# Performance work log

Hardware: AMD Instinct MI355X
Metric: run time of the kernel (lower is better)

## Reference

```python
import jax, jax.numpy as jnp
import numpy as np

DIM, NWIN, TOPK, HEADS = 128, 8, 4, 4
SCALE = DIM ** -0.5


def conv2d(x, w, groups=1, pad=0):
    return jax.lax.conv_general_dilated(
        x, w, (1, 1), [(pad, pad), (pad, pad)],
        feature_group_count=groups,
        dimension_numbers=('NCHW', 'OIHW', 'NCHW'))


def to_windows(elem):
    # elem: [b, C, H, W] -> [b, n_hw, hs, ws, C]
    b, c, h, w = elem.shape
    hs, ws = h // NWIN, w // NWIN
    y = elem.transpose(0, 2, 3, 1)                       # b H W C
    y = y.reshape(b, NWIN, hs, NWIN, ws, c)
    y = y.transpose(0, 1, 3, 2, 4, 5)                    # b n_h n_w hs ws C
    return y.reshape(b, NWIN * NWIN, hs, ws, c)


def from_windows(out, hs, ws):
    # out: [b, n_hw, s_hw, C] -> [b, H, W, C]
    b, nw, s, c = out.shape
    y = out.reshape(b, NWIN, NWIN, hs, ws, c)
    y = y.transpose(0, 1, 3, 2, 4, 5)
    return y.reshape(b, NWIN * hs, NWIN * ws, c)


def window_attention(elem, mlp_w, mlp_b):
    # elem: [b, 3*dim, H, W]
    b, c3, h, w = elem.shape
    hs, ws = h // NWIN, w // NWIN
    win = to_windows(elem)                               # b n_hw hs ws 3C
    q = win[..., :DIM]                                   # b n_hw hs ws C
    kv = win[..., DIM:]                                  # b n_hw hs ws 2C
    nw, s = NWIN * NWIN, hs * ws
    q_pix = q.reshape(b, nw, s, DIM)
    kv_pix = kv.reshape(b, nw, s, 2 * DIM)
    # window-level 'max' projection (WinProj)
    q_win = jax.lax.stop_gradient(q_pix.max(axis=2))             # b nw C
    k_win = jax.lax.stop_gradient(kv_pix[..., :DIM].max(axis=2))  # b nw C
    # top-k routing (diff_routing=False, mul_weight='none' -> only indices used)
    logits = jnp.einsum('bic,bjc->bij', q_win * SCALE, k_win)    # b nw nw
    _, r_idx = jax.lax.top_k(logits, TOPK)                       # b nw topk
    # gather selected kv windows: b nw topk s 2C
    kv_sel = jax.vmap(lambda kvb, ib: kvb[ib])(kv_pix, r_idx)
    kv_sel = kv_sel.reshape(b, nw, TOPK * s, 2 * DIM)
    k_sel = kv_sel[..., :DIM].reshape(b, nw, TOPK * s, HEADS, DIM // HEADS)
    v_sel = kv_sel[..., DIM:].reshape(b, nw, TOPK * s, HEADS, DIM // HEADS)
    qh = q_pix.reshape(b, nw, s, HEADS, DIM // HEADS)
    attn = jnp.einsum('bwshd,bwthd->bwhst', qh * SCALE, k_sel)
    attn = jax.nn.softmax(attn, axis=-1)
    out = jnp.einsum('bwhst,bwthd->bwshd', attn, v_sel)
    out = out.reshape(b, nw, s, DIM)
    out = from_windows(out, hs, ws)                      # b H W C
    out = jnp.einsum('bhwi,oi->bhwo', out, mlp_w) + mlp_b
    return out.transpose(0, 3, 1, 2)                     # b C H W


def setup_inputs() -> dict:
    key = jax.random.key(0)
    ks = jax.random.split(key, 12)
    d = DIM
    return {
        'x': jax.random.normal(ks[0], (1, d, 128, 128), jnp.float32),
        'qkv2_w': jax.random.normal(ks[1], (3 * d, d, 1, 1), jnp.float32) * 0.05,
        'dw3_w': jax.random.normal(ks[2], (3 * d, 1, 3, 3), jnp.float32) * 0.1,
        'pw3_w': jax.random.normal(ks[3], (3 * d, (3 * d) // (3 * HEADS), 1, 1), jnp.float32) * 0.05,
        'dw5_w': jax.random.normal(ks[4], (3 * d, 1, 5, 5), jnp.float32) * 0.1,
        'pw5_w': jax.random.normal(ks[5], (3 * d, (3 * d) // (3 * HEADS), 1, 1), jnp.float32) * 0.05,
        'mlp_w': jax.random.normal(ks[6], (d, d), jnp.float32) * 0.05,
        'mlp_b': jnp.zeros((d,), jnp.float32),
        'proj_w': jax.random.normal(ks[7], (d, 3 * d, 1, 1), jnp.float32) * 0.05,
        'ln_g': jnp.ones((d,), jnp.float32),
        'ln_b': jnp.zeros((d,), jnp.float32),
    }


def reference(x, qkv2_w, dw3_w, pw3_w, dw5_w, pw5_w, mlp_w, mlp_b, proj_w, ln_g, ln_b):
    qkv = conv2d(x, qkv2_w)                              # b 3C H W
    branches = [qkv]
    for dw, pw, k in ((dw3_w, pw3_w, 3), (dw5_w, pw5_w, 5)):
        y = conv2d(qkv, dw, groups=3 * DIM, pad=k // 2)  # depthwise
        y = conv2d(y, pw, groups=3 * HEADS)              # grouped 1x1
        branches.append(y)
    outs = [window_attention(e, mlp_w, mlp_b) for e in branches]
    out = jnp.concatenate(outs, axis=1)                  # b 3C H W
    out = conv2d(out, proj_w)                            # b C H W
    # ln2d: LayerNorm over channel dim
    mu = out.mean(axis=1, keepdims=True)
    var = out.var(axis=1, keepdims=True)
    out = (out - mu) * jax.lax.rsqrt(var + 1e-5)
    out = out * ln_g[None, :, None, None] + ln_b[None, :, None, None]
    return out
```

## Files before the change

kernel.cpp:

```cpp
#include <hip/hip_runtime.h>
#include <math.h>

#define P 16384
#define SCALEF 0.08838834764831845f
#define QSCALE 0.12752075616290145f

typedef short bf16x8 __attribute__((ext_vector_type(8)));
typedef float f32x4 __attribute__((ext_vector_type(4)));

__device__ __forceinline__ unsigned short f2bf(float x) {
  union { float f; unsigned int u; } v; v.f = x;
  unsigned int r = v.u + 0x7fffu + ((v.u >> 16) & 1u);
  return (unsigned short)(r >> 16);
}
__device__ __forceinline__ unsigned int packbf(float a, float b) {
  return (unsigned int)f2bf(a) | ((unsigned int)f2bf(b) << 16);
}
__device__ __forceinline__ unsigned int pr2(float a, float b) {
  union { float f; unsigned int u; } ua, ub; ua.f = a; ub.f = b;
  return __builtin_amdgcn_perm(ub.u + 0x8000u, ua.u + 0x8000u, 0x07060302u);
}
__device__ __forceinline__ unsigned int pk2(float a, float b) {
  unsigned int r;
  asm("v_cvt_pk_bf16_f32 %0, %1, %2" : "=v"(r) : "v"(a), "v"(b));
  return r;
}
#define EXP2F(x) __builtin_amdgcn_exp2f(x)

template<int NS, int JT>
__global__ __launch_bounds__(256) void k_conv_mfma(
    const float* __restrict__ in, const float* __restrict__ w,
    const float* __restrict__ bias, float* __restrict__ out,
    const int IC, const int in_zstr, const int out_zstr)
{
  const int p0  = blockIdx.x * (JT * 64);
  const int oc0 = blockIdx.y * 64;
  in  += (size_t)blockIdx.z * (size_t)in_zstr;
  out += (size_t)blockIdx.z * (size_t)out_zstr;
  const int tid = threadIdx.x;
  const int wv = tid >> 6;
  const int lane = tid & 63;
  const int qi = lane & 15, g = lane >> 4;

  __shared__ __align__(16) unsigned int bS[NS][JT * 64 * 16];
  __shared__ __align__(16) unsigned int aS[NS][64 * 16];

  const f32x4 fz = {0.f, 0.f, 0.f, 0.f};
  f32x4 acc[JT][4];
  #pragma unroll
  for (int j = 0; j < JT; ++j)
    #pragma unroll
    for (int o = 0; o < 4; ++o) acc[j][o] = fz;

  for (int k0 = 0; k0 < IC; k0 += 32) {
    __syncthreads();
    {
      const int kB = tid >> 4;
      const int pB = (tid & 15) * (JT * 4);
      const float* r0 = in + (size_t)(k0 + 2 * kB) * P + p0 + pB;
      #pragma unroll
      for (int half = 0; half < JT / 2; ++half) {
        float x0[8], x1[8];
        #pragma unroll
        for (int v = 0; v < 2; ++v) {
          float4 a = ((const float4*)r0)[half * 2 + v];
          float4 c = ((const float4*)(r0 + P))[half * 2 + v];
          x0[4*v] = a.x; x0[4*v+1] = a.y; x0[4*v+2] = a.z; x0[4*v+3] = a.w;
          x1[4*v] = c.x; x1[4*v+1] = c.y; x1[4*v+2] = c.z; x1[4*v+3] = c.w;
        }
        #pragma unroll
        for (int ii = 0; ii < 8; ++ii) {
          const int i8 = (ii + tid) & 7;
          const int i = half * 8 + i8;
          const unsigned idx = (unsigned)((pB + i) * 16 + (kB ^ ((i & 3) << 2)));
          const unsigned u0 = __float_as_uint(x0[i8]);
          const unsigned u1 = __float_as_uint(x1[i8]);
          bS[0][idx] = __builtin_amdgcn_perm(u1, u0, 0x07060302u);
          const float r0f = x0[i8] - __uint_as_float(u0 & 0xffff0000u);
          const float r1f = x1[i8] - __uint_as_float(u1 & 0xffff0000u);
          bS[1][idx] = pr2(r0f, r1f);
        }
      }
    }
    {
      const int oA = tid >> 2;
      const int kA = (tid & 3) * 8;
      const float* rw = w + (size_t)(oc0 + oA) * IC + k0 + kA;
      float4 wa = ((const float4*)rw)[0];
      float4 wb = ((const float4*)rw)[1];
      float y[8] = {wa.x, wa.y, wa.z, wa.w, wb.x, wb.y, wb.z, wb.w};
      #pragma unroll
      for (int i = 0; i < 4; ++i) {
        const int dd = (kA >> 1) + i;
        const unsigned idx = (unsigned)(oA * 16 + (dd ^ ((oA & 3) << 2)));
        const unsigned u0 = __float_as_uint(y[2*i]);
        const unsigned u1 = __float_as_uint(y[2*i+1]);
        aS[0][idx] = __builtin_amdgcn_perm(u1, u0, 0x07060302u);
        const float r0f = y[2*i]   - __uint_as_float(u0 & 0xffff0000u);
        const float r1f = y[2*i+1] - __uint_as_float(u1 & 0xffff0000u);
        aS[1][idx] = pr2(r0f, r1f);
      }
    }
    __syncthreads();

    bf16x8 aF[4][NS];
    #pragma unroll
    for (int o = 0; o < 4; ++o) {
      const unsigned ab = (unsigned)((o * 16 + qi) * 16 + 4 * (g ^ (qi & 3)));
      #pragma unroll
      for (int s = 0; s < NS; ++s)
        aF[o][s] = *(const bf16x8*)&aS[s][ab];
    }
    #pragma unroll
    for (int j = 0; j < JT; ++j) {
      const unsigned bb = (unsigned)(((wv * JT + j) * 16 + qi) * 16 + 4 * (g ^ (qi & 3)));
      const bf16x8 b0 = *(const bf16x8*)&bS[0][bb];
      const bf16x8 b1 = *(const bf16x8*)&bS[1][bb];
      #pragma unroll
      for (int o = 0; o < 4; ++o) {
        acc[j][o] = __builtin_amdgcn_mfma_f32_16x16x32_bf16(aF[o][0], b0, acc[j][o], 0, 0, 0);
        acc[j][o] = __builtin_amdgcn_mfma_f32_16x16x32_bf16(aF[o][0], b1, acc[j][o], 0, 0, 0);
        acc[j][o] = __builtin_amdgcn_mfma_f32_16x16x32_bf16(aF[o][1], b0, acc[j][o], 0, 0, 0);
      }
    }
  }

  float bv[4][4];
  #pragma unroll
  for (int o = 0; o < 4; ++o)
    #pragma unroll
    for (int t = 0; t < 4; ++t)
      bv[o][t] = bias ? bias[oc0 + o * 16 + 4 * g + t] : 0.f;

  #pragma unroll
  for (int j = 0; j < JT; ++j) {
    const int px = p0 + (wv * JT + j) * 16 + qi;
    #pragma unroll
    for (int o = 0; o < 4; ++o)
      #pragma unroll
      for (int t = 0; t < 4; ++t)
        out[(size_t)(oc0 + o * 16 + 4 * g + t) * P + px] = acc[j][o][t] + bv[o][t];
  }
}

__global__ __launch_bounds__(256) void k_projln(
    const float* __restrict__ in, const float* __restrict__ w,
    const float* __restrict__ bias, const float* __restrict__ ln_g,
    const float* __restrict__ ln_b, float* __restrict__ out)
{
  const int p0 = blockIdx.x * 64;
  const int tid = threadIdx.x;
  const int wv = tid >> 6;
  const int lane = tid & 63;
  const int qi = lane & 15, g = lane >> 4;

  __shared__ __align__(16) unsigned int bS[2][64 * 16];
  __shared__ __align__(16) unsigned int aS[2][128 * 16];

  const f32x4 fz = {0.f, 0.f, 0.f, 0.f};
  f32x4 acc[8];
  #pragma unroll
  for (int o = 0; o < 8; ++o) acc[o] = fz;

  for (int k0 = 0; k0 < 384; k0 += 32) {
    __syncthreads();
    {
      const int kB = tid >> 4;
      const int pB = (tid & 15) * 4;
      const float* r0 = in + (size_t)(k0 + 2 * kB) * P + p0 + pB;
      float4 a = *(const float4*)r0;
      float4 c = *(const float4*)(r0 + P);
      const float x0[4] = {a.x, a.y, a.z, a.w};
      const float x1[4] = {c.x, c.y, c.z, c.w};
      #pragma unroll
      for (int i = 0; i < 4; ++i) {
        const unsigned idx = (unsigned)((pB + i) * 16 + (kB ^ (i << 2)));
        const unsigned u0 = __float_as_uint(x0[i]);
        const unsigned u1 = __float_as_uint(x1[i]);
        bS[0][idx] = __builtin_amdgcn_perm(u1, u0, 0x07060302u);
        const float r0f = x0[i] - __uint_as_float(u0 & 0xffff0000u);
        const float r1f = x1[i] - __uint_as_float(u1 & 0xffff0000u);
        bS[1][idx] = pr2(r0f, r1f);
      }
    }
    {
      const int oA = tid >> 1;
      const int kA = (tid & 1) * 16;
      const float* rw = w + (size_t)oA * 384 + k0 + kA;
      float4 wa = ((const float4*)rw)[0];
      float4 wb = ((const float4*)rw)[1];
      float4 wc = ((const float4*)rw)[2];
      float4 wd = ((const float4*)rw)[3];
      const float y[16] = {wa.x, wa.y, wa.z, wa.w, wb.x, wb.y, wb.z, wb.w,
                           wc.x, wc.y, wc.z, wc.w, wd.x, wd.y, wd.z, wd.w};
      #pragma unroll
      for (int i = 0; i < 8; ++i) {
        const int dd = (kA >> 1) + i;
        const unsigned idx = (unsigned)(oA * 16 + (dd ^ ((oA & 3) << 2)));
        const unsigned u0 = __float_as_uint(y[2*i]);
        const unsigned u1 = __float_as_uint(y[2*i+1]);
        aS[0][idx] = __builtin_amdgcn_perm(u1, u0, 0x07060302u);
        const float r0f = y[2*i]   - __uint_as_float(u0 & 0xffff0000u);
        const float r1f = y[2*i+1] - __uint_as_float(u1 & 0xffff0000u);
        aS[1][idx] = pr2(r0f, r1f);
      }
    }
    __syncthreads();

    const unsigned bb = (unsigned)((wv * 16 + qi) * 16 + 4 * (g ^ (qi & 3)));
    const bf16x8 b0 = *(const bf16x8*)&bS[0][bb];
    const bf16x8 b1 = *(const bf16x8*)&bS[1][bb];
    #pragma unroll
    for (int o = 0; o < 8; ++o) {
      const unsigned ab = (unsigned)((o * 16 + qi) * 16 + 4 * (g ^ (qi & 3)));
      const bf16x8 a0 = *(const bf16x8*)&aS[0][ab];
      const bf16x8 a1 = *(const bf16x8*)&aS[1][ab];
      acc[o] = __builtin_amdgcn_mfma_f32_16x16x32_bf16(a0, b0, acc[o], 0, 0, 0);
      acc[o] = __builtin_amdgcn_mfma_f32_16x16x32_bf16(a0, b1, acc[o], 0, 0, 0);
      acc[o] = __builtin_amdgcn_mfma_f32_16x16x32_bf16(a1, b0, acc[o], 0, 0, 0);
    }
  }

  const int px = p0 + wv * 16 + qi;
  float vch[8][4];
  float sum = 0.f, sq = 0.f;
  #pragma unroll
  for (int o = 0; o < 8; ++o)
    #pragma unroll
    for (int t = 0; t < 4; ++t) {
      const float v = acc[o][t] + bias[o * 16 + 4 * g + t];
      vch[o][t] = v; sum += v; sq += v * v;
    }
  sum += __shfl_xor(sum, 16, 64); sum += __shfl_xor(sum, 32, 64);
  sq  += __shfl_xor(sq, 16, 64);  sq  += __shfl_xor(sq, 32, 64);
  const float mu = sum * (1.f / 128.f);
  const float var = sq * (1.f / 128.f) - mu * mu;
  const float rs = rsqrtf(var + 1e-5f);
  #pragma unroll
  for (int o = 0; o < 8; ++o)
    #pragma unroll
    for (int t = 0; t < 4; ++t) {
      const int oc = o * 16 + 4 * g + t;
      out[(size_t)oc * P + px] = (vch[o][t] - mu) * rs * ln_g[oc] + ln_b[oc];
    }
}

__global__ __launch_bounds__(128) void k_fold(
    const float* __restrict__ proj_w, const float* __restrict__ mlp_w,
    const float* __restrict__ mlp_b, float* __restrict__ Wc,
    float* __restrict__ bc)
{
  const int o = blockIdx.x;
  const int b = blockIdx.y;
  const int i = threadIdx.x;
  const float* pw = proj_w + o * 384 + b * 128;
  float acc = 0.f;
  for (int j = 0; j < 128; ++j)
    acc += pw[j] * mlp_w[j * 128 + i];
  Wc[o * 384 + b * 128 + i] = acc;
  if (b == 0) {
    const float* pwo = proj_w + o * 384;
    float s = (pwo[i] + pwo[i + 128] + pwo[i + 256]) * mlp_b[i];
    #pragma unroll
    for (int sh = 1; sh <= 32; sh <<= 1) s += __shfl_xor(s, sh, 64);
    __shared__ float r2[2];
    if ((i & 63) == 0) r2[i >> 6] = s;
    __syncthreads();
    if (i == 0) bc[o] = r2[0] + r2[1];
  }
}

__global__ __launch_bounds__(256) void k_dwf(
    const float* __restrict__ in, const float* __restrict__ w3,
    const float* __restrict__ w5, float* __restrict__ out3,
    float* __restrict__ out5)
{
  const int c  = blockIdx.y;
  const int ty = blockIdx.x;
  const int y0 = ty * 16;
  __shared__ float tS[20][136];
  const float* ip = in + (size_t)c * P;

  if (threadIdx.x < 20) {
    tS[threadIdx.x][0] = 0.f; tS[threadIdx.x][1] = 0.f;
    tS[threadIdx.x][130] = 0.f; tS[threadIdx.x][131] = 0.f;
  }
  for (int e = threadIdx.x; e < 640; e += 256) {
    const int r = e >> 5, q = e & 31;
    const int gy = y0 + r - 2;
    float4 v = make_float4(0.f, 0.f, 0.f, 0.f);
    if (gy >= 0 && gy < 128) v = *(const float4*)&ip[gy * 128 + q * 4];
    *(float4*)&tS[r][2 + q * 4] = v;
  }
  __syncthreads();

  float a3[9], a5[25];
  #pragma unroll
  for (int i = 0; i < 9; ++i)  a3[i] = w3[c * 9 + i];
  #pragma unroll
  for (int i = 0; i < 25; ++i) a5[i] = w5[c * 25 + i];

  const int py  = threadIdx.x >> 4;
  const int px0 = (threadIdx.x & 15) * 8;
  float o3[8] = {}, o5[8] = {};
  #pragma unroll
  for (int r = 0; r < 5; ++r) {
    float4 sa = *(const float4*)&tS[py + r][px0];
    float4 sb = *(const float4*)&tS[py + r][px0 + 4];
    float4 sc = *(const float4*)&tS[py + r][px0 + 8];
    const float s[12] = {sa.x, sa.y, sa.z, sa.w, sb.x, sb.y, sb.z, sb.w,
                         sc.x, sc.y, sc.z, sc.w};
    #pragma unroll
    for (int j = 0; j < 8; ++j) {
      float acc = a5[r * 5 + 0] * s[j];
      #pragma unroll
      for (int d = 1; d < 5; ++d) acc += a5[r * 5 + d] * s[j + d];
      o5[j] += acc;
    }
    if (r >= 1 && r <= 3) {
      #pragma unroll
      for (int j = 0; j < 8; ++j) {
        float b = a3[(r - 1) * 3 + 0] * s[j + 1];
        b += a3[(r - 1) * 3 + 1] * s[j + 2];
        b += a3[(r - 1) * 3 + 2] * s[j + 3];
        o3[j] += b;
      }
    }
  }
  const size_t ob = (size_t)c * P + (y0 + py) * 128 + px0;
  float4* p3 = (float4*)&out3[ob];
  float4* p5 = (float4*)&out5[ob];
  p3[0] = make_float4(o3[0], o3[1], o3[2], o3[3]);
  p3[1] = make_float4(o3[4], o3[5], o3[6], o3[7]);
  p5[0] = make_float4(o5[0], o5[1], o5[2], o5[3]);
  p5[1] = make_float4(o5[4], o5[5], o5[6], o5[7]);
}

__global__ __launch_bounds__(256) void k_pw2(
    const float* in0, const float* __restrict__ w0, float* out0,
    const float* in1, const float* __restrict__ w1, float* out1)
{
  const float* in = blockIdx.z ? in1 : in0;
  const float* w  = blockIdx.z ? w1 : w0;
  float*      out = blockIdx.z ? out1 : out0;
  const int g = blockIdx.y;
  const int p = blockIdx.x * 256 + threadIdx.x;
  __shared__ float wL[1024];
  for (int e = threadIdx.x; e < 1024; e += 256) wL[e] = w[g * 1024 + e];
  __syncthreads();
  float r[32];
  #pragma unroll
  for (int i = 0; i < 32; ++i) r[i] = in[(g * 32 + i) * P + p];
  #pragma unroll
  for (int o = 0; o < 32; ++o) {
    float acc = 0.f;
    #pragma unroll
    for (int i = 0; i < 32; ++i) acc += wL[o * 32 + i] * r[i];
    out[(g * 32 + o) * P + p] = acc;
  }
}

__global__ __launch_bounds__(256) void k_topk(
    const float* __restrict__ qwin, const float* __restrict__ kwin,
    int* __restrict__ ridx)
{
  const int b = blockIdx.y;
  const int i = blockIdx.x * 4 + (threadIdx.x >> 6);
  const int j = threadIdx.x & 63;
  const float4* q4 = (const float4*)&qwin[(b * 64 + i) * 128];
  const float4* k4 = (const float4*)&kwin[(b * 64 + j) * 128];
  float v = 0.f;
  #pragma unroll
  for (int t = 0; t < 32; ++t) {
    float4 a = q4[t], c = k4[t];
    v += a.x * c.x + a.y * c.y + a.z * c.z + a.w * c.w;
  }
  int res[4];
  #pragma unroll
  for (int r = 0; r < 4; ++r) {
    float bv = v; int bj = j;
    #pragma unroll
    for (int s = 1; s < 64; s <<= 1) {
      const float ov = __shfl_xor(bv, s, 64);
      const int   oj = __shfl_xor(bj, s, 64);
      if (ov > bv || (ov == bv && oj < bj)) { bv = ov; bj = oj; }
    }
    res[r] = bj;
    if (j == bj) v = -INFINITY;
  }
  if (j == 0)
    *(int4*)&ridx[(b * 64 + i) * 4] = make_int4(res[0], res[1], res[2], res[3]);
}

__global__ __launch_bounds__(256) void k_repack(
    const float* __restrict__ e0, const float* __restrict__ e1,
    const float* __restrict__ e2, unsigned int* __restrict__ kvimg,
    unsigned int* __restrict__ qimg, float* __restrict__ qwin,
    float* __restrict__ kwin)
{
  const int fl = blockIdx.x + 64 * (blockIdx.y + 4 * blockIdx.z);
  const int nf = (fl & 7) * 96 + (fl >> 3);
  const int w = nf & 63, h = (nf >> 6) & 3, b = nf >> 8;
  const float* e = (b == 0) ? e0 : ((b == 1) ? e1 : e2);
  const int wy = w >> 3, wx = w & 7;
  const int jbase = wy * 16 * 128 + wx * 16;
  const int t = threadIdx.x;
  unsigned int* kwin_img = kvimg + (size_t)((b * 4 + h) * 64 + w) * 8192;
  unsigned int* qwin_img = qimg  + (size_t)((b * 4 + h) * 64 + w) * 4096;

  __shared__ float redS[32][257];
  __shared__ float part[8][32];
  float kreg[32];

  {
    const int key = t;
    const int hw = jbase + (key >> 4) * 128 + (key & 15);
    const float* eK = e + (size_t)(128 + h * 32) * P + hw;
    const float* eQ = e + (size_t)(h * 32) * P + hw;
    const int half = key >> 7, kl = key & 127;
    unsigned int* kd = kwin_img + half * 4096 + kl * 16;
    unsigned int* qd = qwin_img + key * 16;
    #pragma unroll
    for (int dd = 0; dd < 16; ++dd) {
      float k0 = eK[(size_t)(2 * dd) * P], k1 = eK[(size_t)(2 * dd + 1) * P];
      kd[dd ^ ((kl & 3) << 2)] = packbf(k0, k1);
      kreg[2 * dd] = k0; kreg[2 * dd + 1] = k1;
      float q0 = eQ[(size_t)(2 * dd) * P];
      float q1 = eQ[(size_t)(2 * dd + 1) * P];
      redS[2 * dd][key] = q0; redS[2 * dd + 1][key] = q1;
      qd[dd] = packbf(q0 * QSCALE, q1 * QSCALE);
    }
  }
  {
    const int half = t >> 7, tt = t & 127;
    const int d = tt >> 2;
    const int kp0 = (tt & 3) * 16;
    const float* eV = e + (size_t)(256 + h * 32 + d) * P;
    unsigned int* vd = kwin_img + half * 4096 + 2048 + d * 64;
    #pragma unroll
    for (int i = 0; i < 16; ++i) {
      const int kp2 = kp0 + i;
      const int key = half * 128 + kp2 * 2;
      const int hw = jbase + (key >> 4) * 128 + (key & 15);
      float v0 = eV[hw], v1 = eV[hw + 1];
      vd[kp2 ^ ((d & 7) << 2)] = packbf(v0, v1);
    }
  }
  __syncthreads();
  {
    const int ch = t & 31, seg = t >> 5;
    float mx = redS[ch][seg * 32];
    #pragma unroll
    for (int i = 1; i < 32; ++i) mx = fmaxf(mx, redS[ch][seg * 32 + i]);
    part[seg][ch] = mx;
  }
  __syncthreads();
  if (t < 32) {
    float mx = part[0][t];
    #pragma unroll
    for (int s = 1; s < 8; ++s) mx = fmaxf(mx, part[s][t]);
    qwin[(size_t)(b * 64 + w) * 128 + h * 32 + t] = mx;
  }
  #pragma unroll
  for (int d = 0; d < 32; ++d) redS[d][t] = kreg[d];
  __syncthreads();
  {
    const int ch = t & 31, seg = t >> 5;
    float mx = redS[ch][seg * 32];
    #pragma unroll
    for (int i = 1; i < 32; ++i) mx = fmaxf(mx, redS[ch][seg * 32 + i]);
    part[seg][ch] = mx;
  }
  __syncthreads();
  if (t < 32) {
    float mx = part[0][t];
    #pragma unroll
    for (int s = 1; s < 8; ++s) mx = fmaxf(mx, part[s][t]);
    kwin[(size_t)(b * 64 + w) * 128 + h * 32 + t] = mx;
  }
}

__global__ __launch_bounds__(512, 4) void k_attn_mfma(
    const unsigned int* __restrict__ kvimg, const unsigned int* __restrict__ qimg,
    const int* __restrict__ ridx, float* __restrict__ attnch)
{
  const int fl = blockIdx.x + 64 * (blockIdx.y + 4 * blockIdx.z);
  const int nf = (fl & 7) * 96 + (fl >> 3);
  const int w = nf & 63, h = (nf >> 6) & 3, b = nf >> 8;
  const int tid = threadIdx.x;
  const int wv = tid >> 6, lane = tid & 63;
  const int qi = lane & 15, g = lane >> 4;
  const int wy = w >> 3, wx = w & 7;

  __shared__ __align__(16) unsigned int kvbuf[2][4096];

  const unsigned int* kwin = kvimg + (size_t)((b * 4 + h) * 64) * 8192;
  const unsigned int* qwin = qimg + (size_t)((b * 4 + h) * 64 + w) * 4096;

  bf16x8 qv[2];
  #pragma unroll
  for (int s = 0; s < 2; ++s) {
    union { uint4 u; bf16x8 v; } tq;
    tq.u = *(const uint4*)(qwin + ((wv * 2 + s) * 16 + qi) * 16 + g * 4);
    qv[s] = tq.v;
  }
  const int4 jv = *(const int4*)(ridx + (b * 64 + w) * 4);
  const int ja[4] = {jv.x, jv.y, jv.z, jv.w};

  const f32x4 fz = {0.f, 0.f, 0.f, 0.f};
  float m[2], l[2];
  f32x4 acc[2][2];
  #pragma unroll
  for (int s = 0; s < 2; ++s) {
    m[s] = -3.0e38f; l[s] = 0.f; acc[s][0] = fz; acc[s][1] = fz;
  }

  uint4 st0, st1;
  {
    const uint4* s4 = (const uint4*)(kwin + (size_t)ja[0] * 8192);
    st0 = s4[tid]; st1 = s4[512 + tid];
  }

#define SOFTMAX_PACK(SC, S, PB) {                                           \
    float wmax = -3.0e38f;                                                  \
    _Pragma("unroll") for (int c = 0; c < 4; ++c)                           \
      _Pragma("unroll") for (int u = 0; u < 2; ++u)                         \
        _Pragma("unroll") for (int t2 = 0; t2 < 4; ++t2)                    \
          wmax = fmaxf(wmax, SC[c][u][t2]);                                 \
    wmax = fmaxf(wmax, __shfl_xor(wmax, 16, 64));                           \
    wmax = fmaxf(wmax, __shfl_xor(wmax, 32, 64));                           \
    const float mnew = fmaxf(m[S], wmax);                                   \
    const float corr = EXP2F(m[S] - mnew);                                  \
    m[S] = mnew;                                                            \
    acc[S][0] *= corr; acc[S][1] *= corr;                                   \
    float psum = 0.f;                                                       \
    _Pragma("unroll") for (int c = 0; c < 4; ++c)                           \
      _Pragma("unroll") for (int u = 0; u < 2; ++u) {                       \
        const float p0 = EXP2F(SC[c][u][0] - mnew);                         \
        const float p1 = EXP2F(SC[c][u][1] - mnew);                         \
        const float p2 = EXP2F(SC[c][u][2] - mnew);                         \
        const float p3 = EXP2F(SC[c][u][3] - mnew);                         \
        psum += (p0 + p1) + (p2 + p3);                                      \
        PB[c][2 * u]     = pk2(p0, p1);                                     \
        PB[c][2 * u + 1] = pk2(p2, p3);                                     \
      }                                                                     \
    l[S] = l[S] * corr + psum;                                              \
  }

  for (int ch = 0; ch < 8; ++ch) {
    {
      uint4* d4 = (uint4*)kvbuf[ch & 1];
      d4[tid] = st0; d4[512 + tid] = st1;
    }
    if (ch < 7) {
      const int nx = ch + 1;
      const uint4* s4 = (const uint4*)(kwin + (size_t)ja[nx >> 1] * 8192
                                       + (size_t)(nx & 1) * 4096);
      st0 = s4[tid]; st1 = s4[512 + tid];
    }
    __syncthreads();

    const unsigned int* bc = kvbuf[ch & 1];
    const bf16x8* kp = (const bf16x8*)bc;
    const unsigned short* vsh = (const unsigned short*)(bc + 2048);

    f32x4 scA[4][2], scB[4][2];
    __builtin_amdgcn_s_setprio(1);
    #pragma unroll
    for (int c = 0; c < 4; ++c) {
      #pragma unroll
      for (int u = 0; u < 2; ++u) {
        const int key = 32 * c + 8 * (qi >> 2) + 4 * u + (qi & 3);
        const bf16x8 ka = kp[key * 4 + (g ^ (qi & 3))];
        scA[c][u] = __builtin_amdgcn_mfma_f32_16x16x32_bf16(ka, qv[0], fz, 0, 0, 0);
        scB[c][u] = __builtin_amdgcn_mfma_f32_16x16x32_bf16(ka, qv[1], fz, 0, 0, 0);
      }
    }
    __builtin_amdgcn_s_setprio(0);
    unsigned int pbA[4][4], pbB[4][4];
    SOFTMAX_PACK(scA, 0, pbA);
    SOFTMAX_PACK(scB, 1, pbB);
    __builtin_amdgcn_s_setprio(1);
    #pragma unroll
    for (int c = 0; c < 4; ++c) {
      #pragma unroll
      for (int dt = 0; dt < 2; ++dt) {
        const int d0 = dt * 16 + qi;
        const bf16x8 va = *(const bf16x8*)&vsh[
            (unsigned)((d0 * 128 + 32 * c + 8 * g) ^ ((d0 & 7) << 3))];
        union { unsigned int u4[4]; bf16x8 v; } pva, pvb;
        pva.u4[0] = pbA[c][0]; pva.u4[1] = pbA[c][1];
        pva.u4[2] = pbA[c][2]; pva.u4[3] = pbA[c][3];
        pvb.u4[0] = pbB[c][0]; pvb.u4[1] = pbB[c][1];
        pvb.u4[2] = pbB[c][2]; pvb.u4[3] = pbB[c][3];
        acc[0][dt] = __builtin_amdgcn_mfma_f32_16x16x32_bf16(va, pva.v, acc[0][dt], 0, 0, 0);
        acc[1][dt] = __builtin_amdgcn_mfma_f32_16x16x32_bf16(va, pvb.v, acc[1][dt], 0, 0, 0);
      }
    }
    __builtin_amdgcn_s_setprio(0);
  }
#undef SOFTMAX_PACK

  #pragma unroll
  for (int s = 0; s < 2; ++s) {
    float lsum = l[s];
    lsum += __shfl_xor(lsum, 16, 64);
    lsum += __shfl_xor(lsum, 32, 64);
    const float inv = 1.f / lsum;
    const int hwq = (wy * 16 + wv * 2 + s) * 128 + wx * 16 + qi;
    #pragma unroll
    for (int dt = 0; dt < 2; ++dt)
      #pragma unroll
      for (int t = 0; t < 4; ++t) {
        const int d = dt * 16 + 4 * g + t;
        attnch[(size_t)(b * 128 + h * 32 + d) * P + hwq] = acc[s][dt][t] * inv;
      }
  }
}

extern "C" void kernel_launch(void* const* d_in, const int* in_sizes, int n_in,
                              void* d_out, int out_size, void* d_ws, size_t ws_size,
                              hipStream_t stream)
{
  (void)in_sizes; (void)n_in; (void)out_size;
  const float* x      = (const float*)d_in[0];
  const float* qkv2_w = (const float*)d_in[1];
  const float* dw3_w  = (const float*)d_in[2];
  const float* pw3_w  = (const float*)d_in[3];
  const float* dw5_w  = (const float*)d_in[4];
  const float* pw5_w  = (const float*)d_in[5];
  const float* mlp_w  = (const float*)d_in[6];
  const float* mlp_b  = (const float*)d_in[7];
  const float* proj_w = (const float*)d_in[8];
  const float* ln_g   = (const float*)d_in[9];
  const float* ln_b   = (const float*)d_in[10];

  float* ws = (float*)d_ws;
  const size_t CH = (size_t)384 * P;
  float* qkv    = ws;
  float* dwt3   = ws + CH;
  float* y3     = ws + 2 * CH;
  float* y5     = ws + 3 * CH;
  float* qwin   = ws + 5 * CH;
  float* kwin   = qwin + 3 * 64 * 128;
  int*   ridx   = (int*)(kwin + 3 * 64 * 128);
  float* Wc     = (float*)(ridx + 768);
  float* bc     = Wc + 128 * 384;
  unsigned int* kvimg = (unsigned int*)(ws + 4 * CH);
  unsigned int* qimg  = (unsigned int*)dwt3;
  float* attnch = y3;
  (void)ws_size;

  k_fold<<<dim3(128, 3), 128, 0, stream>>>(proj_w, mlp_w, mlp_b, Wc, bc);

  k_conv_mfma<2, 2><<<dim3(128, 6, 1), 256, 0, stream>>>(x, qkv2_w, nullptr, qkv, 128, 0, 0);
  k_dwf<<<dim3(8, 384), 256, 0, stream>>>(qkv, dw3_w, dw5_w, dwt3, y5);
  k_pw2<<<dim3(64, 12, 2), 256, 0, stream>>>(dwt3, pw3_w, y3, y5, pw5_w, y5);
  k_repack<<<dim3(64, 4, 3), 256, 0, stream>>>(qkv, y3, y5, kvimg, qimg, qwin, kwin);
  k_topk<<<dim3(16, 3), 256, 0, stream>>>(qwin, kwin, ridx);
  k_attn_mfma<<<dim3(64, 4, 3), 512, 0, stream>>>(kvimg, qimg, ridx, attnch);
  k_projln<<<dim3(256), 256, 0, stream>>>(attnch, Wc, bc, ln_g, ln_b, (float*)d_out);
}
```

Before: 185.3 us.

## Process window pairs in repack for wider coalesced loads; reorder dwf grid

k_repack now has each 512-thread block handle two horizontally adjacent windows. Row reads therefore cover 32 contiguous floats instead of 16, and V is loaded as float4 rows instead of scattered scalar pairs. The max reductions for q and k are staged per window through shared memory in four phases. k_dwf's grid is transposed so consecutive blocks walk channels rather than row tiles, which changes cache and scheduling order. The cost is more barriers, larger register arrays (qreg and kreg) and half as many blocks.

```diff
diff --git a/kernel.cpp b/kernel.cpp
--- a/kernel.cpp
+++ b/kernel.cpp
@@ -275,8 +275,8 @@
     const float* __restrict__ w5, float* __restrict__ out3,
     float* __restrict__ out5)
 {
-  const int c  = blockIdx.y;
-  const int ty = blockIdx.x;
+  const int c  = blockIdx.x;
+  const int ty = blockIdx.y;
   const int y0 = ty * 16;
   __shared__ float tS[20][136];
   const float* ip = in + (size_t)c * P;
@@ -392,91 +392,98 @@
     *(int4*)&ridx[(b * 64 + i) * 4] = make_int4(res[0], res[1], res[2], res[3]);
 }
 
-__global__ __launch_bounds__(256) void k_repack(
+__global__ __launch_bounds__(512) void k_repack(
     const float* __restrict__ e0, const float* __restrict__ e1,
     const float* __restrict__ e2, unsigned int* __restrict__ kvimg,
     unsigned int* __restrict__ qimg, float* __restrict__ qwin,
     float* __restrict__ kwin)
 {
-  const int fl = blockIdx.x + 64 * (blockIdx.y + 4 * blockIdx.z);
-  const int nf = (fl & 7) * 96 + (fl >> 3);
-  const int w = nf & 63, h = (nf >> 6) & 3, b = nf >> 8;
+  const int fl = blockIdx.x + 32 * (blockIdx.y + 4 * blockIdx.z);
+  const int nf = (fl & 7) * 48 + (fl >> 3);
+  const int wp = nf & 31, h = (nf >> 5) & 3, b = nf >> 7;
   const float* e = (b == 0) ? e0 : ((b == 1) ? e1 : e2);
-  const int wy = w >> 3, wx = w & 7;
-  const int jbase = wy * 16 * 128 + wx * 16;
+  const int w0 = wp * 2;
+  const int wy = w0 >> 3, wx0 = w0 & 7;
+  const int jbase0 = (wy * 16) * 128 + wx0 * 16;
   const int t = threadIdx.x;
-  unsigned int* kwin_img = kvimg + (size_t)((b * 4 + h) * 64 + w) * 8192;
-  unsigned int* qwin_img = qimg  + (size_t)((b * 4 + h) * 64 + w) * 4096;
 
   __shared__ float redS[32][257];
-  __shared__ float part[8][32];
-  float kreg[32];
-
+  __shared__ float part[16][32];
+
+  float qreg[32], kreg[32];
+
+  const int row = t >> 5, x = t & 31;
+  const int win = x >> 4, key = row * 16 + (x & 15);
   {
-    const int key = t;
-    const int hw = jbase + (key >> 4) * 128 + (key & 15);
+    const int hw = jbase0 + row * 128 + x;
     const float* eK = e + (size_t)(128 + h * 32) * P + hw;
     const float* eQ = e + (size_t)(h * 32) * P + hw;
     const int half = key >> 7, kl = key & 127;
-    unsigned int* kd = kwin_img + half * 4096 + kl * 16;
-    unsigned int* qd = qwin_img + key * 16;
+    unsigned int* kd = kvimg + (size_t)((b * 4 + h) * 64 + w0 + win) * 8192
+                       + half * 4096 + kl * 16;
+    unsigned int* qd = qimg + (size_t)((b * 4 + h) * 64 + w0 + win) * 4096
+                       + key * 16;
     #pragma unroll
     for (int dd = 0; dd < 16; ++dd) {
       float k0 = eK[(size_t)(2 * dd) * P], k1 = eK[(size_t)(2 * dd + 1) * P];
+      kreg[2 * dd] = k0; kreg[2 * dd + 1] = k1;
       kd[dd ^ ((kl & 3) << 2)] = packbf(k0, k1);
-      kreg[2 * dd] = k0; kreg[2 * dd + 1] = k1;
-      float q0 = eQ[(size_t)(2 * dd) * P];
-      float q1 = eQ[(size_t)(2 * dd + 1) * P];
-      redS[2 * dd][key] = q0; redS[2 * dd + 1][key] = q1;
+      float q0 = eQ[(size_t)(2 * dd) * P], q1 = eQ[(size_t)(2 * dd + 1) * P];
+      qreg[2 * dd] = q0; qreg[2 * dd + 1] = q1;
       qd[dd] = packbf(q0 * QSCALE, q1 * QSCALE);
     }
   }
   {
-    const int half = t >> 7, tt = t & 127;
-    const int d = tt >> 2;
-    const int kp0 = (tt & 3) * 16;
-    const float* eV = e + (size_t)(256 + h * 32 + d) * P;
-    unsigned int* vd = kwin_img + half * 4096 + 2048 + d * 64;
-    #pragma unroll
-    for (int i = 0; i < 16; ++i) {
-      const int kp2 = kp0 + i;
-      const int key = half * 128 + kp2 * 2;
-      const int hw = jbase + (key >> 4) * 128 + (key & 15);
-      float v0 = eV[hw], v1 = eV[hw + 1];
-      vd[kp2 ^ ((d & 7) << 2)] = packbf(v0, v1);
-    }
-  }
-  __syncthreads();
-  {
-    const int ch = t & 31, seg = t >> 5;
-    float mx = redS[ch][seg * 32];
-    #pragma unroll
-    for (int i = 1; i < 32; ++i) mx = fmaxf(mx, redS[ch][seg * 32 + i]);
-    part[seg][ch] = mx;
-  }
-  __syncthreads();
-  if (t < 32) {
-    float mx = part[0][t];
-    #pragma unroll
-    for (int s = 1; s < 8; ++s) mx = fmaxf(mx, part[s][t]);
-    qwin[(size_t)(b * 64 + w) * 128 + h * 32 + t] = mx;
-  }
-  #pragma unroll
-  for (int d = 0; d < 32; ++d) redS[d][t] = kreg[d];
-  __syncthreads();
-  {
-    const int ch = t & 31, seg = t >> 5;
-    float mx = redS[ch][seg * 32];
-    #pragma unroll
-    for (int i = 1; i < 32; ++i) mx = fmaxf(mx, redS[ch][seg * 32 + i]);
-    part[seg][ch] = mx;
-  }
-  __syncthreads();
-  if (t < 32) {
-    float mx = part[0][t];
-    #pragma unroll
-    for (int s = 1; s < 8; ++s) mx = fmaxf(mx, part[s][t]);
-    kwin[(size_t)(b * 64 + w) * 128 + h * 32 + t] = mx;
+    const int vwin = t & 1, r = t >> 1;
+    const int half = r >> 7, d = (r & 127) >> 2, q4 = r & 3;
+    const int R = 8 * half + 2 * q4;
+    const float* eV = e + (size_t)(256 + h * 32 + d) * P + jbase0 + vwin * 16;
+    float rv[2][16];
+    #pragma unroll
+    for (int rr = 0; rr < 2; ++rr) {
+      const float4* src = (const float4*)&eV[(R + rr) * 128];
+      #pragma unroll
+      for (int i = 0; i < 4; ++i) {
+        float4 v = src[i];
+        rv[rr][4*i] = v.x; rv[rr][4*i+1] = v.y;
+        rv[rr][4*i+2] = v.z; rv[rr][4*i+3] = v.w;
+      }
+    }
+    unsigned int* vd = kvimg + (size_t)((b * 4 + h) * 64 + w0 + vwin) * 8192
+                       + half * 4096 + 2048 + d * 64;
+    #pragma unroll
+    for (int j = 0; j < 16; ++j) {
+      const int kp2 = q4 * 16 + j;
+      const int rr = j >> 3, pp = (j & 7) * 2;
+      vd[kp2 ^ ((d & 7) << 2)] = packbf(rv[rr][pp], rv[rr][pp + 1]);
+    }
+  }
+  #pragma unroll
+  for (int ph = 0; ph < 4; ++ph) {
+    const int pwv = ph & 1;
+    const bool isq = ph < 2;
+    __syncthreads();
+    if (win == pwv) {
+      #pragma unroll
+      for (int ch = 0; ch < 32; ++ch)
+        redS[ch][key] = isq ? qreg[ch] : kreg[ch];
+    }
+    __syncthreads();
+    {
+      const int ch = t & 31, seg = t >> 5;
+      float mx = redS[ch][seg * 16];
+      #pragma unroll
+      for (int i = 1; i < 16; ++i) mx = fmaxf(mx, redS[ch][seg * 16 + i]);
+      part[seg][ch] = mx;
+    }
+    __syncthreads();
+    if (t < 32) {
+      float mx = part[0][t];
+      #pragma unroll
+      for (int s = 1; s < 16; ++s) mx = fmaxf(mx, part[s][t]);
+      float* dst = isq ? qwin : kwin;
+      dst[(size_t)(b * 64 + w0 + pwv) * 128 + h * 32 + t] = mx;
+    }
   }
 }
 
@@ -654,9 +661,9 @@
   k_fold<<<dim3(128, 3), 128, 0, stream>>>(proj_w, mlp_w, mlp_b, Wc, bc);
 
   k_conv_mfma<2, 2><<<dim3(128, 6, 1), 256, 0, stream>>>(x, qkv2_w, nullptr, qkv, 128, 0, 0);
-  k_dwf<<<dim3(8, 384), 256, 0, stream>>>(qkv, dw3_w, dw5_w, dwt3, y5);
+  k_dwf<<<dim3(384, 8), 256, 0, stream>>>(qkv, dw3_w, dw5_w, dwt3, y5);
   k_pw2<<<dim3(64, 12, 2), 256, 0, stream>>>(dwt3, pw3_w, y3, y5, pw5_w, y5);
-  k_repack<<<dim3(64, 4, 3), 256, 0, stream>>>(qkv, y3, y5, kvimg, qimg, qwin, kwin);
+  k_repack<<<dim3(32, 4, 3), 512, 0, stream>>>(qkv, y3, y5, kvimg, qimg, qwin, kwin);
   k_topk<<<dim3(16, 3), 256, 0, stream>>>(qwin, kwin, ridx);
   k_attn_mfma<<<dim3(64, 4, 3), 512, 0, stream>>>(kvimg, qimg, ridx, attnch);
   k_projln<<<dim3(256), 256, 0, stream>>>(attnch, Wc, bc, ln_g, ln_b, (float*)d_out);
```

Measured after the change: 185.8 us. Within noise of the previous version (+0.3%).
